# Optimization experiments

Measured on AMD Instinct MI355X. Metric: run time of the kernel, lower is better.

Reference implementation:

```python
import jax, jax.numpy as jnp
import numpy as np

B, T, V, H = 64, 101, 8000, 512
P_DROP = 0.3
EPS = 1e-5


def setup_inputs() -> dict:
    key = jax.random.key(0)
    ks = jax.random.split(key, 20)
    s = 1.0 / np.sqrt(H)
    inp = {
        "x": jax.random.randint(ks[0], (B, T), 0, V),
        "emb": jax.random.normal(ks[1], (V, H), jnp.float32) * 0.1,
        "Wd": jax.random.normal(ks[2], (V, H), jnp.float32) * s,
        "bd": jnp.zeros((V,), jnp.float32),
    }
    for l in range(1, 4):
        k = jax.random.split(ks[2 + l], 4)
        inp[f"Wih{l}"] = jax.random.normal(k[0], (4 * H, H), jnp.float32) * s
        inp[f"Whh{l}"] = jax.random.normal(k[1], (4 * H, H), jnp.float32) * s
        inp[f"b{l}"] = jnp.zeros((4 * H,), jnp.float32)
        inp[f"gamma{l}"] = jnp.ones((H,), jnp.float32)
        inp[f"beta{l}"] = jnp.zeros((H,), jnp.float32)
        # LockedDropout: one mask per sequence, reused at every timestep
        keep = jax.random.bernoulli(k[2], 1.0 - P_DROP, (B, H))
        inp[f"mask{l}"] = keep.astype(jnp.float32) / (1.0 - P_DROP)
    return inp


def _lstm_cell(x, h, c, Wih, Whh, b):
    gates = x @ Wih.T + h @ Whh.T + b  # [B, 4H]
    i, f, g, o = jnp.split(gates, 4, axis=-1)
    c = jax.nn.sigmoid(f) * c + jax.nn.sigmoid(i) * jnp.tanh(g)
    h = jax.nn.sigmoid(o) * jnp.tanh(c)
    return h, c


def _bn_train(h, gamma, beta):
    mu = jnp.mean(h, axis=0)
    var = jnp.mean(jnp.square(h - mu), axis=0)  # biased, as BatchNorm1d train
    return gamma * (h - mu) * jax.lax.rsqrt(var + EPS) + beta


def reference(x, emb, Wd, bd,
              Wih1, Whh1, b1, gamma1, beta1, mask1,
              Wih2, Whh2, b2, gamma2, beta2, mask2,
              Wih3, Whh3, b3, gamma3, beta3, mask3):
    e = emb[x]                      # [B, T, H]
    xs = jnp.swapaxes(e[:, :-1, :], 0, 1)  # [T-1, B, H]
    z = jnp.zeros((B, H), jnp.float32)

    def step(carry, xt):
        h1, c1, h2, c2, h3, c3 = carry
        h1, c1 = _lstm_cell(xt, h1, c1, Wih1, Whh1, b1)
        h = _bn_train(h1, gamma1, beta1) * mask1
        h2, c2 = _lstm_cell(h, h2, c2, Wih2, Whh2, b2)
        h = _bn_train(h2, gamma2, beta2) * mask2
        h3, c3 = _lstm_cell(h, h3, c3, Wih3, Whh3, b3)
        h = _bn_train(h3, gamma3, beta3) * mask3
        logits = h @ Wd.T + bd      # [B, V]
        return (h1, c1, h2, c2, h3, c3), logits

    _, logits = jax.lax.scan(step, (z, z, z, z, z, z), xs)  # [T-1, B, V]

    target_prediction = jnp.swapaxes(logits, 0, 1).reshape(-1, V)  # [B*(T-1), V]
    target = x[:, 1:].reshape(-1)
    logp = jax.nn.log_softmax(target_prediction, axis=-1)
    loss = -jnp.mean(jnp.take_along_axis(logp, target[:, None], axis=1))
    outputs = jnp.transpose(logits, (1, 2, 0))  # [B, V, T-1]
    return loss, outputs
```

## Files before the change

kernel.cpp:

```cpp
#include <hip/hip_runtime.h>
#include <hip/hip_bf16.h>
#include <math.h>

#define NBATCH 64
#define TT 101
#define TM 100
#define VV 8000
#define HH 512
#define H4 2048
#define EPSBN 1e-5f

typedef __attribute__((ext_vector_type(8))) short short8;
typedef __attribute__((ext_vector_type(4))) float floatx4;
typedef unsigned short bfraw;

__device__ __forceinline__ bfraw f2b(float f) {
  __hip_bfloat16 h = __float2bfloat16(f);
  return __builtin_bit_cast(bfraw, h);
}
__device__ __forceinline__ float sigm(float x) { return 1.f / (1.f + expf(-x)); }

__device__ __forceinline__ short8 ld16_coh(const bfraw* p) {
  union { unsigned long long u[2]; short8 v; } r;
  r.u[0] = __hip_atomic_load((const unsigned long long*)p, __ATOMIC_RELAXED,
                             __HIP_MEMORY_SCOPE_AGENT);
  r.u[1] = __hip_atomic_load((const unsigned long long*)p + 1, __ATOMIC_RELAXED,
                             __HIP_MEMORY_SCOPE_AGENT);
  return r.v;
}
__device__ __forceinline__ void st_u32_coh(bfraw* p, unsigned v) {
  __hip_atomic_store((unsigned*)p, v, __ATOMIC_RELAXED, __HIP_MEMORY_SCOPE_AGENT);
}
__device__ __forceinline__ void wait_ge(unsigned* p, unsigned target) {
  while (__hip_atomic_load(p, __ATOMIC_RELAXED, __HIP_MEMORY_SCOPE_AGENT) < target)
    __builtin_amdgcn_s_sleep(2);
}
__device__ __forceinline__ void wait_both(unsigned* p1, unsigned n1,
                                          unsigned* p2, unsigned n2) {
  for (;;) {
    unsigned a = __hip_atomic_load(p1, __ATOMIC_RELAXED, __HIP_MEMORY_SCOPE_AGENT);
    unsigned b = __hip_atomic_load(p2, __ATOMIC_RELAXED, __HIP_MEMORY_SCOPE_AGENT);
    if (a >= n1 && b >= n2) break;
    __builtin_amdgcn_s_sleep(2);
  }
}

#define OFF_XE    0UL
#define OFF_X1    6553600UL
#define OFF_W1I   58982400UL
#define OFF_W1H   61079552UL
#define OFF_W2I   63176704UL
#define OFF_W2H   65273856UL
#define OFF_W3I   67371008UL
#define OFF_W3H   69468160UL
#define OFF_WDB   71565312UL
#define OFF_OUT1  79757312UL
#define OFF_OUT2  86310912UL
#define OFF_H3O   92864512UL
#define OFF_HST   99418112UL
#define OFF_CST   100204544UL
#define OFF_SYNC  100597760UL
#define OFF_DONE  100597824UL
#define OFF_PMAX  100599040UL
#define OFF_PSUM  103799040UL
#define OFF_TLG   106999040UL

__global__ void k_zero(unsigned* p, int n) {
  int i = blockIdx.x * 256 + threadIdx.x;
  if (i < n) p[i] = 0u;
}

__global__ void k_embed(const int* __restrict__ x, const float* __restrict__ emb,
                        bfraw* __restrict__ xe) {
  int t = blockIdx.x >> 6, b = blockIdx.x & 63;
  int idx = x[b * TT + t];
  const float* src = emb + (size_t)idx * HH;
  bfraw* dst = xe + (size_t)blockIdx.x * HH;
  for (int e = threadIdx.x; e < HH; e += 256) dst[e] = f2b(src[e]);
}

__global__ void k_cast(const float* __restrict__ s, bfraw* __restrict__ d, int n) {
  int i = blockIdx.x * 256 + threadIdx.x;
  if (i < n) d[i] = f2b(s[i]);
}

__global__ __launch_bounds__(256) void k_gemm_x1(const bfraw* __restrict__ A,
                                                 const bfraw* __restrict__ Bw,
                                                 const float* __restrict__ bias,
                                                 float* __restrict__ X1) {
  int nb = blockIdx.x, mb = blockIdx.y;
  int tid = threadIdx.x, lane = tid & 63, wv = tid >> 6;
  int l15 = lane & 15, lq = lane >> 4;
  int m0 = mb * 64, n0 = nb * 64;
  floatx4 acc[4];
  for (int nt = 0; nt < 4; nt++) {
    float bv = bias[n0 + nt * 16 + l15];
    floatx4 t = {bv, bv, bv, bv};
    acc[nt] = t;
  }
  int arow = m0 + wv * 16 + l15;
  for (int ks = 0; ks < 16; ++ks) {
    int k = ks * 32 + lq * 8;
    short8 a = *(const short8*)&A[(size_t)arow * HH + k];
#pragma unroll
    for (int nt = 0; nt < 4; nt++) {
      short8 b = *(const short8*)&Bw[(size_t)(n0 + nt * 16 + l15) * HH + k];
      acc[nt] = __builtin_amdgcn_mfma_f32_16x16x32_bf16(a, b, acc[nt], 0, 0, 0);
    }
  }
#pragma unroll
  for (int nt = 0; nt < 4; nt++)
#pragma unroll
    for (int q = 0; q < 4; q++) {
      int m = m0 + wv * 16 + lq * 4 + q;
      X1[(size_t)m * H4 + n0 + nt * 16 + l15] = acc[nt][q];
    }
}

__global__ __launch_bounds__(256, 1) void k_recurrent(
    const float* __restrict__ X1,
    const bfraw* __restrict__ w1h, const bfraw* __restrict__ w2i, const bfraw* __restrict__ w2h,
    const bfraw* __restrict__ w3i, const bfraw* __restrict__ w3h,
    const float* __restrict__ b2, const float* __restrict__ b3,
    const float* __restrict__ g1, const float* __restrict__ be1, const float* __restrict__ mk1,
    const float* __restrict__ g2, const float* __restrict__ be2, const float* __restrict__ mk2,
    const float* __restrict__ g3, const float* __restrict__ be3, const float* __restrict__ mk3,
    bfraw* __restrict__ out1, bfraw* __restrict__ out2, bfraw* __restrict__ h3out,
    bfraw* __restrict__ hst, float* __restrict__ cst,
    unsigned* done) {
  __shared__ __align__(16) bfraw wlds[64 * 520];
  __shared__ __align__(16) float gd[64 * 65];
  __shared__ float stats[32];

  const int bid = blockIdx.x, tid = threadIdx.x;
  const int lane = tid & 63, wv = tid >> 6;
  const int l15 = lane & 15, lq = lane >> 4;

  int layer, cshift, j0;
  if (bid < 32)       { layer = 0; cshift = 4; j0 = bid << 4; }
  else if (bid < 96)  { layer = 1; cshift = 3; j0 = (bid - 32) << 3; }
  else                { layer = 2; cshift = 3; j0 = (bid - 96) << 3; }
  const int cols = 1 << cshift;
  const int NT = (layer == 0) ? 4 : 2;
  const int gstride = 4 * cols + 1;

  const bfraw* wih = (layer == 1) ? w2i : w3i;
  const bfraw* whh = (layer == 0) ? w1h : ((layer == 1) ? w2h : w3h);

  if (layer == 0) {
    for (int r = wv * 16; r < wv * 16 + 16; ++r) {
      int g = r >> 4, jj = r & 15;
      const bfraw* src = whh + (size_t)(g * HH + j0 + jj) * HH;
      *(short8*)&wlds[r * 520 + lane * 8] = *(const short8*)&src[lane * 8];
    }
  } else {
    for (int r2 = wv * 16; r2 < wv * 16 + 16; ++r2) {
      int mat = r2 >> 5, r = r2 & 31;
      int g = r >> 3, jj = r & 7;
      const bfraw* src = (mat ? whh : wih) + (size_t)(g * HH + j0 + jj) * HH;
      *(short8*)&wlds[r2 * 520 + lane * 8] = *(const short8*)&src[lane * 8];
    }
  }
  __syncthreads();

  const float* bb  = (layer == 1) ? b2 : b3;
  const float* gam = (layer == 0) ? g1 : ((layer == 1) ? g2 : g3);
  const float* bet = (layer == 0) ? be1 : ((layer == 1) ? be2 : be3);
  const float* msk = (layer == 0) ? mk1 : ((layer == 1) ? mk2 : mk3);
  bfraw* hbase = hst + (size_t)layer * 2 * NBATCH * HH;
  float* myc = cst + (size_t)layer * NBATCH * HH;

  const unsigned nprev = (layer == 1) ? 32u : 64u;
  const unsigned nself = (layer == 0) ? 32u : 64u;
  unsigned* dprev = done + (layer - 1) * TM;
  unsigned* dself = done + layer * TM;

  for (int t = 0; t < TM; ++t) {
    const bfraw* hr = hbase + (size_t)(t & 1) * NBATCH * HH;
    bfraw* hw = hbase + (size_t)((t + 1) & 1) * NBATCH * HH;
    const bfraw* xin = ((layer == 1) ? out1 : out2) + (size_t)t * NBATCH * HH;

    floatx4 acc[4];
    if (layer == 0) {
      const float* xrow = X1 + (size_t)t * NBATCH * H4;
      int rbase = wv * 16 + lq * 4;
#pragma unroll
      for (int nt = 0; nt < 4; nt++) {
        int colg = nt * HH + j0 + l15;
        acc[nt][0] = xrow[(rbase + 0) * H4 + colg];
        acc[nt][1] = xrow[(rbase + 1) * H4 + colg];
        acc[nt][2] = xrow[(rbase + 2) * H4 + colg];
        acc[nt][3] = xrow[(rbase + 3) * H4 + colg];
      }
    } else {
      floatx4 z = {0.f, 0.f, 0.f, 0.f};
      for (int nt = 0; nt < 4; nt++) acc[nt] = z;
    }

    if (tid == 0) {
      if (layer > 0) {
        if (t > 0) wait_both(dprev + t, nprev, dself + t - 1, nself);
        else       wait_ge(dprev + t, nprev);
      } else if (t > 0) {
        wait_ge(dself + t - 1, nself);
      }
    }
    __syncthreads();

    const int arow = wv * 16 + l15;
    short8 hg[16];
#pragma unroll
    for (int ks = 0; ks < 16; ++ks)
      hg[ks] = ld16_coh(&hr[(size_t)arow * HH + ks * 32 + lq * 8]);
    short8 xg[16];
    if (layer > 0) {
#pragma unroll
      for (int ks = 0; ks < 16; ++ks)
        xg[ks] = ld16_coh(&xin[(size_t)arow * HH + ks * 32 + lq * 8]);
    }

    if (layer == 0) {
#pragma unroll
      for (int ks = 0; ks < 16; ++ks) {
        int k = ks * 32 + lq * 8;
#pragma unroll
        for (int nt = 0; nt < 4; nt++) {
          short8 bh = *(const short8*)&wlds[(nt * 16 + l15) * 520 + k];
          acc[nt] = __builtin_amdgcn_mfma_f32_16x16x32_bf16(hg[ks], bh, acc[nt], 0, 0, 0);
        }
      }
    } else {
#pragma unroll
      for (int ks = 0; ks < 16; ++ks) {
        int k = ks * 32 + lq * 8;
#pragma unroll
        for (int nt = 0; nt < 2; nt++) {
          short8 bx = *(const short8*)&wlds[(nt * 16 + l15) * 520 + k];
          short8 bh = *(const short8*)&wlds[((32 + nt * 16) + l15) * 520 + k];
          acc[nt] = __builtin_amdgcn_mfma_f32_16x16x32_bf16(xg[ks], bx, acc[nt], 0, 0, 0);
          acc[nt] = __builtin_amdgcn_mfma_f32_16x16x32_bf16(hg[ks], bh, acc[nt], 0, 0, 0);
        }
      }
    }
    {
      int rbase = wv * 16 + lq * 4;
      for (int nt = 0; nt < NT; nt++)
#pragma unroll
        for (int q = 0; q < 4; q++)
          gd[(rbase + q) * gstride + nt * 16 + l15] = acc[nt][q];
    }
    __syncthreads();
    const int half = cshift - 1;
    const int ne2 = NBATCH << half;
    for (int e = tid; e < ne2; e += 256) {
      int m = e >> half;
      int jp = (e & ((cols >> 1) - 1)) << 1;
      float hv[2];
#pragma unroll
      for (int u = 0; u < 2; u++) {
        int jj = jp + u, j = j0 + jj;
        float gi = gd[m * gstride + 0 * cols + jj];
        float gf = gd[m * gstride + 1 * cols + jj];
        float gg = gd[m * gstride + 2 * cols + jj];
        float go = gd[m * gstride + 3 * cols + jj];
        if (layer) { gi += bb[j]; gf += bb[HH + j]; gg += bb[2 * HH + j]; go += bb[3 * HH + j]; }
        float c = sigm(gf) * myc[m * HH + j] + sigm(gi) * tanhf(gg);
        float h = sigm(go) * tanhf(c);
        myc[m * HH + j] = c;
        hv[u] = h;
      }
      unsigned hpack = (unsigned)f2b(hv[0]) | ((unsigned)f2b(hv[1]) << 16);
      st_u32_coh(&hw[m * HH + j0 + jp], hpack);
      gd[m * gstride + jp] = hv[0];
      gd[m * gstride + jp + 1] = hv[1];
    }
    __syncthreads();
    {
      int tpc = 256 >> cshift;
      int c_ = tid >> (8 - cshift), r_ = tid & (tpc - 1);
      float s1 = 0.f, s2 = 0.f;
      for (int m = r_; m < NBATCH; m += tpc) {
        float v = gd[m * gstride + c_];
        s1 += v; s2 += v * v;
      }
      for (int off = 1; off < tpc; off <<= 1) {
        s1 += __shfl_xor(s1, off);
        s2 += __shfl_xor(s2, off);
      }
      if (r_ == 0) {
        float mu = s1 * (1.f / NBATCH);
        float var = s2 * (1.f / NBATCH) - mu * mu;
        stats[c_ * 2] = mu;
        stats[c_ * 2 + 1] = rsqrtf(var + EPSBN);
      }
    }
    __syncthreads();
    for (int e = tid; e < ne2; e += 256) {
      int m = e >> half;
      int jp = (e & ((cols >> 1) - 1)) << 1;
      float ov[2];
#pragma unroll
      for (int u = 0; u < 2; u++) {
        int jj = jp + u, j = j0 + jj;
        float h = gd[m * gstride + jj];
        ov[u] = (gam[j] * ((h - stats[jj * 2]) * stats[jj * 2 + 1]) + bet[j]) * msk[m * HH + j];
      }
      unsigned opack = (unsigned)f2b(ov[0]) | ((unsigned)f2b(ov[1]) << 16);
      if (layer == 0)
        st_u32_coh(&out1[(size_t)(t * NBATCH + m) * HH + j0 + jp], opack);
      else if (layer == 1)
        st_u32_coh(&out2[(size_t)(t * NBATCH + m) * HH + j0 + jp], opack);
      else
        *(unsigned*)&h3out[((size_t)m * TM + t) * HH + j0 + jp] = opack;
    }
    __builtin_amdgcn_s_waitcnt(0);
    __syncthreads();
    if (tid == 0)
      __hip_atomic_fetch_add(dself + t, 1u, __ATOMIC_RELAXED, __HIP_MEMORY_SCOPE_AGENT);
  }
}

__global__ __launch_bounds__(256) void k_dec(const bfraw* __restrict__ A,
                                             const bfraw* __restrict__ Bw,
                                             const float* __restrict__ bd,
                                             const int* __restrict__ x,
                                             float* __restrict__ out,
                                             float* __restrict__ pmax,
                                             float* __restrict__ psum,
                                             float* __restrict__ tlg) {
  __shared__ __align__(16) float tb[64 * 65];
  int nb = blockIdx.x, mb = blockIdx.y;
  int tid = threadIdx.x, lane = tid & 63, wv = tid >> 6;
  int l15 = lane & 15, lq = lane >> 4;
  int m0 = mb * 64, n0 = nb * 64;
  floatx4 acc[4];
  for (int nt = 0; nt < 4; nt++) {
    float bv = bd[n0 + nt * 16 + l15];
    floatx4 t = {bv, bv, bv, bv};
    acc[nt] = t;
  }
  int arow = m0 + wv * 16 + l15;
  for (int ks = 0; ks < 16; ++ks) {
    int k = ks * 32 + lq * 8;
    short8 a = *(const short8*)&A[(size_t)arow * HH + k];
#pragma unroll
    for (int nt = 0; nt < 4; nt++) {
      short8 b = *(const short8*)&Bw[(size_t)(n0 + nt * 16 + l15) * HH + k];
      acc[nt] = __builtin_amdgcn_mfma_f32_16x16x32_bf16(a, b, acc[nt], 0, 0, 0);
    }
  }
#pragma unroll
  for (int q = 0; q < 4; q++) {
    float mx = fmaxf(fmaxf(acc[0][q], acc[1][q]), fmaxf(acc[2][q], acc[3][q]));
    for (int off = 1; off < 16; off <<= 1) mx = fmaxf(mx, __shfl_xor(mx, off));
    float sm = expf(acc[0][q] - mx) + expf(acc[1][q] - mx) +
               expf(acc[2][q] - mx) + expf(acc[3][q] - mx);
    for (int off = 1; off < 16; off <<= 1) sm += __shfl_xor(sm, off);
    if (l15 == 0) {
      int m = m0 + wv * 16 + lq * 4 + q;
      pmax[(size_t)m * 125 + nb] = mx;
      psum[(size_t)m * 125 + nb] = sm;
    }
  }
  {
    int rbase = wv * 16 + lq * 4;
#pragma unroll
    for (int nt = 0; nt < 4; nt++)
#pragma unroll
      for (int q = 0; q < 4; q++)
        tb[(rbase + q) * 65 + nt * 16 + l15] = acc[nt][q];
  }
  __syncthreads();
  int ml = tid & 63, vq = tid >> 6;
  int m = m0 + ml;
  int b = m / TM, t = m - b * TM;
  int tgt = x[b * TT + t + 1];
  float* obase = out + (size_t)b * VV * TM + t;
  for (int i = 0; i < 16; ++i) {
    int cv = vq * 16 + i;
    int v = n0 + cv;
    float val = tb[ml * 65 + cv];
    obase[(size_t)v * TM] = val;
    if (v == tgt) tlg[m] = val;
  }
}

__global__ void k_loss(const float* __restrict__ pmax, const float* __restrict__ psum,
                       const float* __restrict__ tlg, float* acc) {
  int m = blockIdx.x * 4 + (threadIdx.x >> 6);
  int lane = threadIdx.x & 63;
  float mx = -3.4e38f;
  for (int i = lane; i < 125; i += 64) mx = fmaxf(mx, pmax[(size_t)m * 125 + i]);
  for (int off = 1; off < 64; off <<= 1) mx = fmaxf(mx, __shfl_xor(mx, off));
  float s = 0.f;
  for (int i = lane; i < 125; i += 64)
    s += psum[(size_t)m * 125 + i] * expf(pmax[(size_t)m * 125 + i] - mx);
  for (int off = 1; off < 64; off <<= 1) s += __shfl_xor(s, off);
  if (lane == 0) atomicAdd(acc, mx + logf(s) - tlg[m]);
}

__global__ void k_final(const float* acc, float* out) { out[0] = acc[0] * (1.f / 6400.f); }

extern "C" void kernel_launch(void* const* d_in, const int* in_sizes, int n_in,
                              void* d_out, int out_size, void* d_ws, size_t ws_size,
                              hipStream_t stream) {
  (void)in_sizes; (void)n_in; (void)out_size; (void)ws_size;
  const int*   x    = (const int*)  d_in[0];
  const float* emb  = (const float*)d_in[1];
  const float* Wd   = (const float*)d_in[2];
  const float* bd   = (const float*)d_in[3];
  const float* Wih1 = (const float*)d_in[4];
  const float* Whh1 = (const float*)d_in[5];
  const float* b1   = (const float*)d_in[6];
  const float* g1   = (const float*)d_in[7];
  const float* be1  = (const float*)d_in[8];
  const float* mk1  = (const float*)d_in[9];
  const float* Wih2 = (const float*)d_in[10];
  const float* Whh2 = (const float*)d_in[11];
  const float* b2   = (const float*)d_in[12];
  const float* g2   = (const float*)d_in[13];
  const float* be2  = (const float*)d_in[14];
  const float* mk2  = (const float*)d_in[15];
  const float* Wih3 = (const float*)d_in[16];
  const float* Whh3 = (const float*)d_in[17];
  const float* b3   = (const float*)d_in[18];
  const float* g3   = (const float*)d_in[19];
  const float* be3  = (const float*)d_in[20];
  const float* mk3  = (const float*)d_in[21];

  char* ws = (char*)d_ws;
  bfraw* XE   = (bfraw*)(ws + OFF_XE);
  float* X1   = (float*)(ws + OFF_X1);
  bfraw* W1I  = (bfraw*)(ws + OFF_W1I);
  bfraw* W1H  = (bfraw*)(ws + OFF_W1H);
  bfraw* W2I  = (bfraw*)(ws + OFF_W2I);
  bfraw* W2H  = (bfraw*)(ws + OFF_W2H);
  bfraw* W3I  = (bfraw*)(ws + OFF_W3I);
  bfraw* W3H  = (bfraw*)(ws + OFF_W3H);
  bfraw* WDB  = (bfraw*)(ws + OFF_WDB);
  bfraw* OUT1 = (bfraw*)(ws + OFF_OUT1);
  bfraw* OUT2 = (bfraw*)(ws + OFF_OUT2);
  bfraw* H3O  = (bfraw*)(ws + OFF_H3O);
  bfraw* HST  = (bfraw*)(ws + OFF_HST);
  float* CST  = (float*)(ws + OFF_CST);
  float* LACC = (float*)(ws + OFF_SYNC);
  unsigned* DONE = (unsigned*)(ws + OFF_DONE);
  float* PMAX = (float*)(ws + OFF_PMAX);
  float* PSUM = (float*)(ws + OFF_PSUM);
  float* TLG  = (float*)(ws + OFF_TLG);

  int zwords = (int)((OFF_PMAX - OFF_HST) / 4);
  k_zero<<<(zwords + 255) / 256, 256, 0, stream>>>((unsigned*)(ws + OFF_HST), zwords);

  k_embed<<<6400, 256, 0, stream>>>(x, emb, XE);

  const int nw = H4 * HH;
  k_cast<<<(nw + 255) / 256, 256, 0, stream>>>(Wih1, W1I, nw);
  k_cast<<<(nw + 255) / 256, 256, 0, stream>>>(Whh1, W1H, nw);
  k_cast<<<(nw + 255) / 256, 256, 0, stream>>>(Wih2, W2I, nw);
  k_cast<<<(nw + 255) / 256, 256, 0, stream>>>(Whh2, W2H, nw);
  k_cast<<<(nw + 255) / 256, 256, 0, stream>>>(Wih3, W3I, nw);
  k_cast<<<(nw + 255) / 256, 256, 0, stream>>>(Whh3, W3H, nw);
  const int nwd = VV * HH;
  k_cast<<<(nwd + 255) / 256, 256, 0, stream>>>(Wd, WDB, nwd);

  k_gemm_x1<<<dim3(32, 100), 256, 0, stream>>>(XE, W1I, b1, X1);

  k_recurrent<<<160, 256, 0, stream>>>(X1, W1H, W2I, W2H, W3I, W3H, b2, b3,
                                       g1, be1, mk1, g2, be2, mk2, g3, be3, mk3,
                                       OUT1, OUT2, H3O, HST, CST, DONE);

  k_dec<<<dim3(125, 100), 256, 0, stream>>>(H3O, WDB, bd, x, ((float*)d_out) + 1,
                                            PMAX, PSUM, TLG);

  k_loss<<<1600, 256, 0, stream>>>(PMAX, PSUM, TLG, LACC);
  k_final<<<1, 1, 0, stream>>>(LACC, (float*)d_out);
}
```

Measured before the change: 2.283 ms.

## Split recurrent done flags into hidden-state and output counters; batch coherent loads via asm

The single per-layer done counter is split into two. One counter signals that the hidden state is written, and it is now raised right after the h/c update, before the batch-norm output stage. The other signals that the layer output is ready. This lets the next timestep of the same layer start without waiting for the BN/dropout output writes, shortening the serial critical path of the recurrence. The coherent 16-byte loads are also replaced with inline-asm global_load_dwordx4 using sc1 and immediate offsets, followed by a single vmcnt wait, so all loads are issued before any is waited on. The risk lies in the new ODONE offset inside the zeroed region and in correctness of the relaxed-ordering handshake.

```diff
diff --git a/kernel.cpp b/kernel.cpp
--- a/kernel.cpp
+++ b/kernel.cpp
@@ -20,14 +20,6 @@
 }
 __device__ __forceinline__ float sigm(float x) { return 1.f / (1.f + expf(-x)); }
 
-__device__ __forceinline__ short8 ld16_coh(const bfraw* p) {
-  union { unsigned long long u[2]; short8 v; } r;
-  r.u[0] = __hip_atomic_load((const unsigned long long*)p, __ATOMIC_RELAXED,
-                             __HIP_MEMORY_SCOPE_AGENT);
-  r.u[1] = __hip_atomic_load((const unsigned long long*)p + 1, __ATOMIC_RELAXED,
-                             __HIP_MEMORY_SCOPE_AGENT);
-  return r.v;
-}
 __device__ __forceinline__ void st_u32_coh(bfraw* p, unsigned v) {
   __hip_atomic_store((unsigned*)p, v, __ATOMIC_RELAXED, __HIP_MEMORY_SCOPE_AGENT);
 }
@@ -44,6 +36,20 @@
     __builtin_amdgcn_s_sleep(2);
   }
 }
+
+#define GLD4(dst, base, OFFS) \
+  asm volatile("global_load_dwordx4 %0, %1, off offset:" OFFS " sc1" \
+               : "=&v"(dst) : "v"(base))
+#define LD16(a, base) do { \
+  GLD4(a[0],  base, "0");   GLD4(a[1],  base, "64");  \
+  GLD4(a[2],  base, "128"); GLD4(a[3],  base, "192"); \
+  GLD4(a[4],  base, "256"); GLD4(a[5],  base, "320"); \
+  GLD4(a[6],  base, "384"); GLD4(a[7],  base, "448"); \
+  GLD4(a[8],  base, "512"); GLD4(a[9],  base, "576"); \
+  GLD4(a[10], base, "640"); GLD4(a[11], base, "704"); \
+  GLD4(a[12], base, "768"); GLD4(a[13], base, "832"); \
+  GLD4(a[14], base, "896"); GLD4(a[15], base, "960"); \
+} while (0)
 
 #define OFF_XE    0UL
 #define OFF_X1    6553600UL
@@ -58,6 +64,7 @@
 #define OFF_OUT2  86310912UL
 #define OFF_H3O   92864512UL
 #define OFF_HST   99418112UL
+#define OFF_ODONE 99811328UL
 #define OFF_CST   100204544UL
 #define OFF_SYNC  100597760UL
 #define OFF_DONE  100597824UL
@@ -127,7 +134,7 @@
     const float* __restrict__ g3, const float* __restrict__ be3, const float* __restrict__ mk3,
     bfraw* __restrict__ out1, bfraw* __restrict__ out2, bfraw* __restrict__ h3out,
     bfraw* __restrict__ hst, float* __restrict__ cst,
-    unsigned* done) {
+    unsigned* hdone, unsigned* odone) {
   __shared__ __align__(16) bfraw wlds[64 * 520];
   __shared__ __align__(16) float gd[64 * 65];
   __shared__ float stats[32];
@@ -172,8 +179,9 @@
 
   const unsigned nprev = (layer == 1) ? 32u : 64u;
   const unsigned nself = (layer == 0) ? 32u : 64u;
-  unsigned* dprev = done + (layer - 1) * TM;
-  unsigned* dself = done + layer * TM;
+  unsigned* oprev = odone + (layer - 1) * TM;
+  unsigned* hself = hdone + layer * TM;
+  unsigned* oself = odone + layer * TM;
 
   for (int t = 0; t < TM; ++t) {
     const bfraw* hr = hbase + (size_t)(t & 1) * NBATCH * HH;
@@ -198,26 +206,26 @@
     }
 
     if (tid == 0) {
-      if (layer > 0) {
-        if (t > 0) wait_both(dprev + t, nprev, dself + t - 1, nself);
-        else       wait_ge(dprev + t, nprev);
-      } else if (t > 0) {
-        wait_ge(dself + t - 1, nself);
+      if (layer == 0) {
+        if (t > 0) wait_ge(hself + t - 1, nself);
+      } else {
+        if (t > 0) wait_both(oprev + t, nprev, hself + t - 1, nself);
+        else       wait_ge(oprev + t, nprev);
       }
     }
     __syncthreads();
 
     const int arow = wv * 16 + l15;
+    const bfraw* ph = hr + (size_t)arow * HH + lq * 8;
     short8 hg[16];
-#pragma unroll
-    for (int ks = 0; ks < 16; ++ks)
-      hg[ks] = ld16_coh(&hr[(size_t)arow * HH + ks * 32 + lq * 8]);
+    LD16(hg, ph);
     short8 xg[16];
     if (layer > 0) {
-#pragma unroll
-      for (int ks = 0; ks < 16; ++ks)
-        xg[ks] = ld16_coh(&xin[(size_t)arow * HH + ks * 32 + lq * 8]);
-    }
+      const bfraw* px = xin + (size_t)arow * HH + lq * 8;
+      LD16(xg, px);
+    }
+    asm volatile("s_waitcnt vmcnt(0)" ::: "memory");
+    __builtin_amdgcn_sched_barrier(0);
 
     if (layer == 0) {
 #pragma unroll
@@ -274,7 +282,10 @@
       gd[m * gstride + jp] = hv[0];
       gd[m * gstride + jp + 1] = hv[1];
     }
+    __builtin_amdgcn_s_waitcnt(0);
     __syncthreads();
+    if (tid == 0)
+      __hip_atomic_fetch_add(hself + t, 1u, __ATOMIC_RELAXED, __HIP_MEMORY_SCOPE_AGENT);
     {
       int tpc = 256 >> cshift;
       int c_ = tid >> (8 - cshift), r_ = tid & (tpc - 1);
@@ -313,10 +324,12 @@
       else
         *(unsigned*)&h3out[((size_t)m * TM + t) * HH + j0 + jp] = opack;
     }
-    __builtin_amdgcn_s_waitcnt(0);
-    __syncthreads();
-    if (tid == 0)
-      __hip_atomic_fetch_add(dself + t, 1u, __ATOMIC_RELAXED, __HIP_MEMORY_SCOPE_AGENT);
+    if (layer < 2) {
+      __builtin_amdgcn_s_waitcnt(0);
+      __syncthreads();
+      if (tid == 0)
+        __hip_atomic_fetch_add(oself + t, 1u, __ATOMIC_RELAXED, __HIP_MEMORY_SCOPE_AGENT);
+    }
   }
 }
 
@@ -444,7 +457,8 @@
   bfraw* HST  = (bfraw*)(ws + OFF_HST);
   float* CST  = (float*)(ws + OFF_CST);
   float* LACC = (float*)(ws + OFF_SYNC);
-  unsigned* DONE = (unsigned*)(ws + OFF_DONE);
+  unsigned* HDONE = (unsigned*)(ws + OFF_DONE);
+  unsigned* ODONE = (unsigned*)(ws + OFF_ODONE);
   float* PMAX = (float*)(ws + OFF_PMAX);
   float* PSUM = (float*)(ws + OFF_PSUM);
   float* TLG  = (float*)(ws + OFF_TLG);
@@ -468,7 +482,7 @@
 
   k_recurrent<<<160, 256, 0, stream>>>(X1, W1H, W2I, W2H, W3I, W3H, b2, b3,
                                        g1, be1, mk1, g2, be2, mk2, g3, be3, mk3,
-                                       OUT1, OUT2, H3O, HST, CST, DONE);
+                                       OUT1, OUT2, H3O, HST, CST, HDONE, ODONE);
 
   k_dec<<<dim3(125, 100), 256, 0, stream>>>(H3O, WDB, bd, x, ((float*)d_out) + 1,
                                             PMAX, PSUM, TLG);
```

Result: faster. 1.831 ms (-19.8%).
